# Optimization experiments

Measured on AMD Instinct MI355X. Metric: run time of the kernel, lower is better.

The kernel has to match this reference:

```python
import jax, jax.numpy as jnp
import numpy as np

EPS = 1e-7  # keras.backend.epsilon()
R_ITER = 3

def _squash(v, axis=-1):
    s2 = jnp.sum(jnp.square(v), axis=axis, keepdims=True)
    scale = s2 / (1.0 + s2) / jnp.sqrt(s2 + EPS)
    return scale * v

def setup_inputs() -> dict:
    key = jax.random.key(0)
    k1, k2 = jax.random.split(key)
    B, J, Din = 64, 2048, 16   # batch, input_n_capsules, input_dim_capsule
    C, Dout = 32, 32           # n_capsules, out_dim_capsule
    x = jax.random.normal(k1, (B, J, Din), dtype=jnp.float32)
    # glorot-uniform-like init for W [C, J, Dout, Din]
    limit = np.sqrt(6.0 / (Din + Dout)).astype(np.float32)
    W = jax.random.uniform(k2, (C, J, Dout, Din), dtype=jnp.float32, minval=-limit, maxval=limit)
    return {"x": x, "W": W}

def reference(x, W):
    # u_hat[b,c,j,o] = sum_i W[c,j,o,i] * x[b,j,i]
    u_hat = jnp.einsum('bji,cjoi->bcjo', x, W)
    B, C, J, _ = u_hat.shape
    b = jnp.zeros((B, C, J), dtype=u_hat.dtype)
    v = None
    for i in range(R_ITER):
        c = jax.nn.softmax(b, axis=1)               # softmax over output capsules (axis=1, as in source)
        s = jnp.einsum('bcj,bcjo->bco', c, u_hat)   # weighted sum over input capsules
        v = _squash(s, axis=-1)                     # [B, C, Dout]
        if i < R_ITER - 1:
            b = b + jnp.einsum('bco,bcjo->bcj', v, u_hat)
    return v
```

## Files before the change

kernel.cpp:

```cpp
#include <hip/hip_runtime.h>
#include <hip/hip_bf16.h>
#include <stdint.h>

#define BB 64
#define JJ 2048
#define DI 16
#define CC 32
#define OO 32
#define CO 1024
#define TJ 16
#define NJT 128

static const size_t W2_BYTES = (size_t)CC * JJ * OO * DI * 2;
static const size_t X3_BYTES = (size_t)BB * JJ * DI * 2;

typedef _Float16 f16x4 __attribute__((ext_vector_type(4)));
typedef float    f32x4 __attribute__((ext_vector_type(4)));
typedef unsigned short ushort_t;

#if defined(__HIP_DEVICE_COMPILE__)
# if __has_builtin(__builtin_amdgcn_mfma_f32_16x16x16f16)
#  define MFMA16(a, b, c) __builtin_amdgcn_mfma_f32_16x16x16f16((a), (b), (c), 0, 0, 0)
# else
#  define MFMA16(a, b, c) __builtin_amdgcn_mfma_f32_16x16x16_f16((a), (b), (c), 0, 0, 0)
# endif
# define SCHED_FENCE() __builtin_amdgcn_sched_barrier(0)
#else
# define MFMA16(a, b, c) (c)
# define SCHED_FENCE()
#endif

#if __has_attribute(amdgpu_waves_per_eu)
# define WAVES4 __attribute__((amdgpu_waves_per_eu(4, 4)))
#else
# define WAVES4
#endif

union Pack2 { unsigned u; _Float16 h[2]; };

__device__ __forceinline__ ushort_t f2bf(float f) {
  unsigned u = __float_as_uint(f);
  u += 0x7FFFu + ((u >> 16) & 1u);
  return (ushort_t)(u >> 16);
}
__device__ __forceinline__ float bf2f(ushort_t b) {
  return __uint_as_float(((unsigned)b) << 16);
}

__global__ __launch_bounds__(256) void prep_w(const float* __restrict__ W,
                                              uint2* __restrict__ W2) {
  const int j = blockIdx.x;
  const int tt = threadIdx.x;
#pragma unroll
  for (int r = 0; r < 16; ++r) {
    const int s = r * 256 + tt;
    const int ct = s >> 6, l = s & 63;
    const int co = ct * 16 + (l & 15);
    const int c = co >> 5, o = co & 31;
    const float4 src = ((const float4*)W)[(((size_t)c * JJ + j) * OO + o) * 4 + (l >> 4)];
    Pack2 a, b;
    a.h[0] = (_Float16)src.x; a.h[1] = (_Float16)src.y;
    b.h[0] = (_Float16)src.z; b.h[1] = (_Float16)src.w;
    W2[(size_t)j * 4096 + s] = make_uint2(a.u, b.u);
  }
}

__global__ __launch_bounds__(256) void prep_x(const float* __restrict__ X,
                                              uint2* __restrict__ X3) {
  const unsigned T = blockIdx.x * 256 + threadIdx.x;
  const int l = T & 63, bt = (T >> 6) & 1, j = (T >> 7) & 2047, bq = (int)(T >> 18);
  const int b = bq * 32 + bt * 16 + (l & 15);
  const float4 src = ((const float4*)X)[((size_t)b * JJ + j) * 4 + (l >> 4)];
  Pack2 a, bb;
  a.h[0] = (_Float16)src.x; a.h[1] = (_Float16)src.y;
  bb.h[0] = (_Float16)src.z; bb.h[1] = (_Float16)src.w;
  X3[T] = make_uint2(a.u, bb.u);
}

template<bool HAVE_V>
__global__ __launch_bounds__(1024, 4) WAVES4 void route_mfma(
    const uint4* __restrict__ X3, const uint4* __restrict__ W2,
    const float* __restrict__ vsum, ushort_t* __restrict__ partial)
{
  __shared__ uint4 wbuf[4][2048];
  __shared__ uint4 xbuf[1024];
  __shared__ float lbuf[2][32 * 33];

  const int jt   = blockIdx.x & (NJT - 1);
  const int bq   = blockIdx.x >> 7;
  const int tid  = threadIdx.x;
  const int w    = tid >> 6;
  const int lane = tid & 63;
  const int g    = lane >> 4;
  const int t    = lane & 15;

  unsigned vsh[2][2][2][2];
  if (HAVE_V) {
#pragma unroll
    for (int cc = 0; cc < 2; ++cc)
#pragma unroll
      for (int bt = 0; bt < 2; ++bt)
#pragma unroll
        for (int hh = 0; hh < 2; ++hh)
#pragma unroll
          for (int rp = 0; rp < 2; ++rp) {
            const float* vp = vsum + (size_t)(bq * 32 + bt * 16 + t) * CO
                            + (2 * w + cc) * OO + hh * 16 + 4 * g + 2 * rp;
            Pack2 p; p.h[0] = (_Float16)vp[0]; p.h[1] = (_Float16)vp[1];
            vsh[cc][bt][hh][rp] = p.u;
          }
    asm volatile("s_waitcnt vmcnt(0)" ::: "memory");
  }

  const uint4* wsrc = W2 + (size_t)jt * TJ * 2048;

#define STAGEW(bufidx, slab) do {                                                 \
    const uint4* sp_ = wsrc + (size_t)(slab) * 2048 + w * 128 + lane;             \
    uint4* dp_ = &wbuf[bufidx][w * 128 + lane];                                   \
    _Pragma("unroll")                                                             \
    for (int r_ = 0; r_ < 2; ++r_)                                                \
      __builtin_amdgcn_global_load_lds(                                           \
          (const __attribute__((address_space(1))) void*)(sp_ + r_ * 64),         \
          (__attribute__((address_space(3))) void*)(dp_ + r_ * 64), 16, 0, 0);    \
  } while (0)

  {
    const uint4* xs = X3 + ((size_t)bq * JJ + jt * TJ) * 64 + tid;
    __builtin_amdgcn_global_load_lds(
        (const __attribute__((address_space(1))) void*)xs,
        (__attribute__((address_space(3))) void*)&xbuf[tid], 16, 0, 0);
  }
  STAGEW(0, 0);
  STAGEW(1, 1);
  STAGEW(2, 2);
  asm volatile("s_waitcnt vmcnt(6)" ::: "memory");
  SCHED_FENCE();
  __builtin_amdgcn_s_barrier();

  f32x4 acc[4][2];
#pragma unroll
  for (int k = 0; k < 4; ++k)
#pragma unroll
    for (int bt = 0; bt < 2; ++bt) acc[k][bt] = f32x4{0.f, 0.f, 0.f, 0.f};

  for (int jj = 0; jj < TJ; ++jj) {
    const int bcur = jj & 3;
    if (jj < TJ - 2)       asm volatile("s_waitcnt vmcnt(4)" ::: "memory");
    else if (jj == TJ - 2) asm volatile("s_waitcnt vmcnt(2)" ::: "memory");
    else                   asm volatile("s_waitcnt vmcnt(0)" ::: "memory");
    SCHED_FENCE();
    if (jj + 3 < TJ) STAGEW((jj + 3) & 3, jj + 3);

    const uint2* wb2 = (const uint2*)wbuf[bcur];
    const uint2* xb2 = (const uint2*)xbuf;

    f16x4 bf[2];
#pragma unroll
    for (int bt = 0; bt < 2; ++bt)
      bf[bt] = __builtin_bit_cast(f16x4, xb2[(jj * 2 + bt) * 64 + lane]);
    f16x4 af[4];
#pragma unroll
    for (int k = 0; k < 4; ++k)
      af[k] = __builtin_bit_cast(f16x4, wb2[(w * 4 + k) * 64 + lane]);

    f32x4 uh[4][2];
#pragma unroll
    for (int k = 0; k < 4; ++k)
#pragma unroll
      for (int bt = 0; bt < 2; ++bt) {
        if (HAVE_V) uh[k][bt] = MFMA16(af[k], bf[bt], (f32x4{0.f, 0.f, 0.f, 0.f}));
        else        acc[k][bt] = MFMA16(af[k], bf[bt], acc[k][bt]);
      }

    if (HAVE_V) {
      float lp[2][2];
#pragma unroll
      for (int cc = 0; cc < 2; ++cc)
#pragma unroll
        for (int bt = 0; bt < 2; ++bt) {
          float s = 0.f;
#pragma unroll
          for (int hh = 0; hh < 2; ++hh)
#pragma unroll
            for (int rp = 0; rp < 2; ++rp) {
              Pack2 p; p.u = vsh[cc][bt][hh][rp];
              s = fmaf(uh[2 * cc + hh][bt][2 * rp],     (float)p.h[0], s);
              s = fmaf(uh[2 * cc + hh][bt][2 * rp + 1], (float)p.h[1], s);
            }
          s += __shfl_xor(s, 16);
          s += __shfl_xor(s, 32);
          lp[cc][bt] = s;
        }
      {
        const float hi = (g & 1) ? lp[1][1] : lp[1][0];
        const float lo = (g & 1) ? lp[0][1] : lp[0][0];
        const float val = (g >> 1) ? hi : lo;
        lbuf[jj & 1][((g & 1) * 16 + t) * 33 + 2 * w + (g >> 1)] = val;
      }
      asm volatile("s_waitcnt lgkmcnt(0)" ::: "memory");
      SCHED_FENCE();
      __builtin_amdgcn_s_barrier();

      {
        const int row = 2 * w + (lane >> 5);
        const int cc2 = lane & 31;
        float e = __expf(lbuf[jj & 1][row * 33 + cc2]);
        float den = e;
        den += __shfl_xor(den, 1);  den += __shfl_xor(den, 2);
        den += __shfl_xor(den, 4);  den += __shfl_xor(den, 8);
        den += __shfl_xor(den, 16);
        lbuf[jj & 1][row * 33 + cc2] = e / den;
      }
      asm volatile("s_waitcnt lgkmcnt(0)" ::: "memory");
      SCHED_FENCE();
      __builtin_amdgcn_s_barrier();

      float cf[2][2];
#pragma unroll
      for (int cc = 0; cc < 2; ++cc)
#pragma unroll
        for (int bt = 0; bt < 2; ++bt)
          cf[cc][bt] = lbuf[jj & 1][(bt * 16 + t) * 33 + 2 * w + cc];
#pragma unroll
      for (int k = 0; k < 4; ++k)
#pragma unroll
        for (int bt = 0; bt < 2; ++bt)
#pragma unroll
          for (int r = 0; r < 4; ++r)
            acc[k][bt][r] = fmaf(cf[k >> 1][bt], uh[k][bt][r], acc[k][bt][r]);
    }
  }
#undef STAGEW

  const float cs = HAVE_V ? 1.f : 0.03125f;
#pragma unroll
  for (int k = 0; k < 4; ++k)
#pragma unroll
    for (int bt = 0; bt < 2; ++bt) {
      const int b  = bq * 32 + bt * 16 + t;
      const int co = (4 * w + k) * 16 + 4 * g;
      ushort4 v;
      v.x = f2bf(acc[k][bt][0] * cs);
      v.y = f2bf(acc[k][bt][1] * cs);
      v.z = f2bf(acc[k][bt][2] * cs);
      v.w = f2bf(acc[k][bt][3] * cs);
      *(ushort4*)(partial + ((size_t)jt * BB + b) * CO + co) = v;
    }
}

template<bool HAVE_V>
__global__ __launch_bounds__(256, 1) void route_f32(
    const float* __restrict__ X, const float* __restrict__ W,
    const float* __restrict__ vsum, float* __restrict__ partial)
{
  const int jt   = blockIdx.x & 63;
  const int bq   = blockIdx.x >> 6;
  const int tid  = threadIdx.x;
  const int wave = tid >> 6;
  const int lane = tid & 63;
  const int c    = lane & 31;
  const int o0   = (lane >> 5) << 4;
  const int b0   = bq * 16 + wave * 4;

  float acc[4][16];
#pragma unroll
  for (int bl = 0; bl < 4; ++bl)
#pragma unroll
    for (int ol = 0; ol < 16; ++ol) acc[bl][ol] = 0.f;

  const float* wbase = W + ((size_t)c * JJ * OO + (size_t)o0) * DI;

  for (int jj = 0; jj < 32; ++jj) {
    const int j = jt * 32 + jj;
    float xf[4][16];
#pragma unroll
    for (int bl = 0; bl < 4; ++bl) {
      const float4* xpt = (const float4*)(X + ((size_t)(b0 + bl) * JJ + j) * DI);
#pragma unroll
      for (int q = 0; q < 4; ++q) {
        float4 x4 = xpt[q];
        xf[bl][4*q+0] = x4.x; xf[bl][4*q+1] = x4.y;
        xf[bl][4*q+2] = x4.z; xf[bl][4*q+3] = x4.w;
      }
    }
    const float4* wp = (const float4*)(wbase + (size_t)j * OO * DI);
    float tv[4][16];
#pragma unroll
    for (int ol = 0; ol < 16; ++ol) {
      float wf[16];
#pragma unroll
      for (int q = 0; q < 4; ++q) {
        float4 w4 = wp[4*ol + q];
        wf[4*q+0] = w4.x; wf[4*q+1] = w4.y;
        wf[4*q+2] = w4.z; wf[4*q+3] = w4.w;
      }
#pragma unroll
      for (int bl = 0; bl < 4; ++bl) {
        float tt = 0.f;
#pragma unroll
        for (int i = 0; i < 16; ++i) tt = fmaf(wf[i], xf[bl][i], tt);
        if (!HAVE_V) acc[bl][ol] += tt;
        else         tv[bl][ol] = tt;
      }
    }
    if (HAVE_V) {
#pragma unroll
      for (int bl = 0; bl < 4; ++bl) {
        float dsum = 0.f;
        const float4* vp = (const float4*)(vsum + (size_t)(b0 + bl) * CO + c * OO + o0);
#pragma unroll
        for (int q = 0; q < 4; ++q) {
          float4 v4 = vp[q];
          dsum = fmaf(v4.x, tv[bl][4*q+0], dsum);
          dsum = fmaf(v4.y, tv[bl][4*q+1], dsum);
          dsum = fmaf(v4.z, tv[bl][4*q+2], dsum);
          dsum = fmaf(v4.w, tv[bl][4*q+3], dsum);
        }
        dsum += __shfl_xor(dsum, 32);
        float mm = dsum;
#pragma unroll
        for (int s = 16; s >= 1; s >>= 1) mm = fmaxf(mm, __shfl_xor(mm, s));
        float e = __expf(dsum - mm);
        float den = e;
#pragma unroll
        for (int s = 16; s >= 1; s >>= 1) den += __shfl_xor(den, s);
        float coef = e / den;
#pragma unroll
        for (int ol = 0; ol < 16; ++ol)
          acc[bl][ol] = fmaf(coef, tv[bl][ol], acc[bl][ol]);
      }
    }
  }
  const float cs = HAVE_V ? 1.f : 0.03125f;
#pragma unroll
  for (int bl = 0; bl < 4; ++bl) {
    float* pp = partial + ((size_t)jt * BB + (b0 + bl)) * CO + c * OO + o0;
#pragma unroll
    for (int q = 0; q < 4; ++q) {
      float4 w4 = make_float4(acc[bl][4*q+0]*cs, acc[bl][4*q+1]*cs,
                              acc[bl][4*q+2]*cs, acc[bl][4*q+3]*cs);
      ((float4*)pp)[q] = w4;
    }
  }
}

__global__ __launch_bounds__(256, 1) void reduce_squash_bf(
    const ushort_t* __restrict__ partial, float* __restrict__ vsum,
    float* __restrict__ out, int mode)
{
  const int idx = blockIdx.x * 256 + threadIdx.x;
  float s0 = 0.f, s1 = 0.f, s2 = 0.f, s3 = 0.f;
#pragma unroll 4
  for (int nt = 0; nt < NJT; nt += 4) {
    s0 += bf2f(partial[(size_t)(nt + 0) * (BB * CO) + idx]);
    s1 += bf2f(partial[(size_t)(nt + 1) * (BB * CO) + idx]);
    s2 += bf2f(partial[(size_t)(nt + 2) * (BB * CO) + idx]);
    s3 += bf2f(partial[(size_t)(nt + 3) * (BB * CO) + idx]);
  }
  float s = (s0 + s1) + (s2 + s3);
  float s2m = s * s;
#pragma unroll
  for (int mk = 16; mk >= 1; mk >>= 1) s2m += __shfl_xor(s2m, mk);
  float scale = s2m / ((1.f + s2m) * sqrtf(s2m + 1e-7f));
  float v = scale * s;
  if (mode == 2)      out[idx] = v;
  else if (mode == 1) vsum[idx] += v;
  else                vsum[idx] = v;
}

template<int NJTR>
__global__ __launch_bounds__(256, 1) void reduce_squash(
    const float* __restrict__ partial, float* __restrict__ vsum,
    float* __restrict__ out, int mode)
{
  const int idx = blockIdx.x * 256 + threadIdx.x;
  float s0 = 0.f, s1 = 0.f, s2 = 0.f, s3 = 0.f;
#pragma unroll 4
  for (int nt = 0; nt < NJTR; nt += 4) {
    s0 += partial[(size_t)(nt + 0) * (BB * CO) + idx];
    s1 += partial[(size_t)(nt + 1) * (BB * CO) + idx];
    s2 += partial[(size_t)(nt + 2) * (BB * CO) + idx];
    s3 += partial[(size_t)(nt + 3) * (BB * CO) + idx];
  }
  float s = (s0 + s1) + (s2 + s3);
  float s2m = s * s;
#pragma unroll
  for (int mk = 16; mk >= 1; mk >>= 1) s2m += __shfl_xor(s2m, mk);
  float scale = s2m / ((1.f + s2m) * sqrtf(s2m + 1e-7f));
  float v = scale * s;
  if (mode == 2)      out[idx] = v;
  else if (mode == 1) vsum[idx] += v;
  else                vsum[idx] = v;
}

static void run_mfma(const float* X, const float* W, float* out,
                     void* d_ws, hipStream_t stream)
{
  uint2* W2         = (uint2*)d_ws;
  uint2* X3         = (uint2*)((char*)d_ws + W2_BYTES);
  ushort_t* partial = (ushort_t*)((char*)d_ws + W2_BYTES + X3_BYTES);
  float* vsum       = (float*)((char*)d_ws + W2_BYTES + X3_BYTES
                               + (size_t)NJT * BB * CO * 2);
  const int grid  = NJT * 2;
  const int rgrid = BB * CO / 256;

  prep_w<<<JJ, 256, 0, stream>>>(W, W2);
  prep_x<<<2048, 256, 0, stream>>>(X, X3);

  route_mfma<false><<<grid, 1024, 0, stream>>>((const uint4*)X3, (const uint4*)W2, nullptr, partial);
  reduce_squash_bf<<<rgrid, 256, 0, stream>>>(partial, vsum, nullptr, 0);

  route_mfma<true><<<grid, 1024, 0, stream>>>((const uint4*)X3, (const uint4*)W2, vsum, partial);
  reduce_squash_bf<<<rgrid, 256, 0, stream>>>(partial, vsum, nullptr, 1);

  route_mfma<true><<<grid, 1024, 0, stream>>>((const uint4*)X3, (const uint4*)W2, vsum, partial);
  reduce_squash_bf<<<rgrid, 256, 0, stream>>>(partial, vsum, out, 2);
}

static void run_f32_fallback(const float* X, const float* W, float* out,
                             void* d_ws, hipStream_t stream)
{
  float* partial = (float*)d_ws;
  float* vsum    = partial + (size_t)64 * BB * CO;
  const int grid  = 64 * 4;
  const int rgrid = BB * CO / 256;

  route_f32<false><<<grid, 256, 0, stream>>>(X, W, nullptr, partial);
  reduce_squash<64><<<rgrid, 256, 0, stream>>>(partial, vsum, nullptr, 0);
  route_f32<true><<<grid, 256, 0, stream>>>(X, W, vsum, partial);
  reduce_squash<64><<<rgrid, 256, 0, stream>>>(partial, vsum, nullptr, 1);
  route_f32<true><<<grid, 256, 0, stream>>>(X, W, vsum, partial);
  reduce_squash<64><<<rgrid, 256, 0, stream>>>(partial, vsum, out, 2);
}

extern "C" void kernel_launch(void* const* d_in, const int* in_sizes, int n_in,
                              void* d_out, int out_size, void* d_ws, size_t ws_size,
                              hipStream_t stream) {
  (void)in_sizes; (void)n_in; (void)out_size;
  const float* X = (const float*)d_in[0];
  const float* W = (const float*)d_in[1];
  float* out = (float*)d_out;

  const size_t need = W2_BYTES + X3_BYTES
                    + (size_t)NJT * BB * CO * 2 + (size_t)BB * CO * 4;
  if (ws_size >= need) run_mfma(X, W, out, d_ws, stream);
  else                 run_f32_fallback(X, W, out, d_ws, stream);
}
```

Before: 148.6 us.

## Fuse W fp16 conversion into first routing pass kernel

Drops the separate prep_w kernel. The first routing iteration now reads fp32 W directly into LDS, converts it to fp16 for the MFMA, and has the blocks with bq==0 write the converted W2 for the later iterations. This removes one full read of the fp32 W (about 134MB) and a kernel launch. In exchange the first pass stages double-size fp32 tiles with only two buffers, and the bq==1 blocks also read fp32 W.

After: 136.9 us. 1.09x faster.

```diff
diff --git a/kernel.cpp b/kernel.cpp
--- a/kernel.cpp
+++ b/kernel.cpp
@@ -47,24 +47,6 @@
   return __uint_as_float(((unsigned)b) << 16);
 }
 
-__global__ __launch_bounds__(256) void prep_w(const float* __restrict__ W,
-                                              uint2* __restrict__ W2) {
-  const int j = blockIdx.x;
-  const int tt = threadIdx.x;
-#pragma unroll
-  for (int r = 0; r < 16; ++r) {
-    const int s = r * 256 + tt;
-    const int ct = s >> 6, l = s & 63;
-    const int co = ct * 16 + (l & 15);
-    const int c = co >> 5, o = co & 31;
-    const float4 src = ((const float4*)W)[(((size_t)c * JJ + j) * OO + o) * 4 + (l >> 4)];
-    Pack2 a, b;
-    a.h[0] = (_Float16)src.x; a.h[1] = (_Float16)src.y;
-    b.h[0] = (_Float16)src.z; b.h[1] = (_Float16)src.w;
-    W2[(size_t)j * 4096 + s] = make_uint2(a.u, b.u);
-  }
-}
-
 __global__ __launch_bounds__(256) void prep_x(const float* __restrict__ X,
                                               uint2* __restrict__ X3) {
   const unsigned T = blockIdx.x * 256 + threadIdx.x;
@@ -77,14 +59,12 @@
   X3[T] = make_uint2(a.u, bb.u);
 }
 
-template<bool HAVE_V>
-__global__ __launch_bounds__(1024, 4) WAVES4 void route_mfma(
-    const uint4* __restrict__ X3, const uint4* __restrict__ W2,
-    const float* __restrict__ vsum, ushort_t* __restrict__ partial)
-{
-  __shared__ uint4 wbuf[4][2048];
+__global__ __launch_bounds__(1024, 4) WAVES4 void route_conv(
+    const uint4* __restrict__ X3, const float* __restrict__ Wf,
+    uint2* __restrict__ W2out, ushort_t* __restrict__ partial)
+{
+  __shared__ uint4 wbuf32[2][4096];
   __shared__ uint4 xbuf[1024];
-  __shared__ float lbuf[2][32 * 33];
 
   const int jt   = blockIdx.x & (NJT - 1);
   const int bq   = blockIdx.x >> 7;
@@ -94,23 +74,129 @@
   const int g    = lane >> 4;
   const int t    = lane & 15;
 
+#define STAGEC(slot, jjv) do {                                                    \
+    const int j_ = jt * TJ + (jjv);                                               \
+    _Pragma("unroll")                                                             \
+    for (int r_ = 0; r_ < 4; ++r_) {                                              \
+      const int ct_ = w * 4 + r_;                                                 \
+      const uint4* sp_ = (const uint4*)Wf                                         \
+          + ((size_t)(ct_ >> 1) * JJ + j_) * 128 + (ct_ & 1) * 64                 \
+          + (lane & 15) * 4 + (lane >> 4);                                        \
+      uint4* dp_ = &wbuf32[slot][w * 256 + r_ * 64 + lane];                       \
+      __builtin_amdgcn_global_load_lds(                                           \
+          (const __attribute__((address_space(1))) void*)sp_,                     \
+          (__attribute__((address_space(3))) void*)dp_, 16, 0, 0);                \
+    }                                                                             \
+  } while (0)
+
+  {
+    const uint4* xs = X3 + ((size_t)bq * JJ + jt * TJ) * 64 + tid;
+    __builtin_amdgcn_global_load_lds(
+        (const __attribute__((address_space(1))) void*)xs,
+        (__attribute__((address_space(3))) void*)&xbuf[tid], 16, 0, 0);
+  }
+  STAGEC(0, 0);
+  STAGEC(1, 1);
+  asm volatile("s_waitcnt vmcnt(8)" ::: "memory");
+  SCHED_FENCE();
+  __builtin_amdgcn_s_barrier();
+
+  f32x4 acc[4][2];
+#pragma unroll
+  for (int k = 0; k < 4; ++k)
+#pragma unroll
+    for (int bt = 0; bt < 2; ++bt) acc[k][bt] = f32x4{0.f, 0.f, 0.f, 0.f};
+
+  for (int jj = 0; jj < TJ; ++jj) {
+    const int bcur = jj & 1;
+    if (jj < TJ - 2) asm volatile("s_waitcnt vmcnt(4)" ::: "memory");
+    else             asm volatile("s_waitcnt vmcnt(0)" ::: "memory");
+    SCHED_FENCE();
+
+    const uint2* xb2 = (const uint2*)xbuf;
+    f16x4 bf[2];
+#pragma unroll
+    for (int bt = 0; bt < 2; ++bt)
+      bf[bt] = __builtin_bit_cast(f16x4, xb2[(jj * 2 + bt) * 64 + lane]);
+
+    const f32x4* wr = (const f32x4*)wbuf32[bcur];
+    f16x4 af[4];
+#pragma unroll
+    for (int k = 0; k < 4; ++k) {
+      f32x4 a32 = wr[w * 256 + k * 64 + lane];
+      af[k][0] = (_Float16)a32[0]; af[k][1] = (_Float16)a32[1];
+      af[k][2] = (_Float16)a32[2]; af[k][3] = (_Float16)a32[3];
+    }
+
+    if (bq == 0) {
+      const size_t wbase = (size_t)(jt * TJ + jj) * 4096;
+#pragma unroll
+      for (int k = 0; k < 4; ++k) {
+        Pack2 p0, p1;
+        p0.h[0] = af[k][0]; p0.h[1] = af[k][1];
+        p1.h[0] = af[k][2]; p1.h[1] = af[k][3];
+        W2out[wbase + (w * 4 + k) * 64 + lane] = make_uint2(p0.u, p1.u);
+      }
+    }
+
+#pragma unroll
+    for (int k = 0; k < 4; ++k)
+#pragma unroll
+      for (int bt = 0; bt < 2; ++bt)
+        acc[k][bt] = MFMA16(af[k], bf[bt], acc[k][bt]);
+
+    asm volatile("s_waitcnt lgkmcnt(0)" ::: "memory");
+    SCHED_FENCE();
+    if (jj + 2 < TJ) STAGEC(bcur, jj + 2);
+  }
+#undef STAGEC
+
+#pragma unroll
+  for (int k = 0; k < 4; ++k)
+#pragma unroll
+    for (int bt = 0; bt < 2; ++bt) {
+      const int b  = bq * 32 + bt * 16 + t;
+      const int co = (4 * w + k) * 16 + 4 * g;
+      ushort4 v;
+      v.x = f2bf(acc[k][bt][0] * 0.03125f);
+      v.y = f2bf(acc[k][bt][1] * 0.03125f);
+      v.z = f2bf(acc[k][bt][2] * 0.03125f);
+      v.w = f2bf(acc[k][bt][3] * 0.03125f);
+      *(ushort4*)(partial + ((size_t)jt * BB + b) * CO + co) = v;
+    }
+}
+
+__global__ __launch_bounds__(1024, 4) WAVES4 void route_v(
+    const uint4* __restrict__ X3, const uint4* __restrict__ W2,
+    const float* __restrict__ vsum, ushort_t* __restrict__ partial)
+{
+  __shared__ uint4 wbuf[4][2048];
+  __shared__ uint4 xbuf[1024];
+  __shared__ float lbuf[2][32 * 33];
+
+  const int jt   = blockIdx.x & (NJT - 1);
+  const int bq   = blockIdx.x >> 7;
+  const int tid  = threadIdx.x;
+  const int w    = tid >> 6;
+  const int lane = tid & 63;
+  const int g    = lane >> 4;
+  const int t    = lane & 15;
+
   unsigned vsh[2][2][2][2];
-  if (HAVE_V) {
-#pragma unroll
-    for (int cc = 0; cc < 2; ++cc)
-#pragma unroll
-      for (int bt = 0; bt < 2; ++bt)
-#pragma unroll
-        for (int hh = 0; hh < 2; ++hh)
-#pragma unroll
-          for (int rp = 0; rp < 2; ++rp) {
-            const float* vp = vsum + (size_t)(bq * 32 + bt * 16 + t) * CO
-                            + (2 * w + cc) * OO + hh * 16 + 4 * g + 2 * rp;
-            Pack2 p; p.h[0] = (_Float16)vp[0]; p.h[1] = (_Float16)vp[1];
-            vsh[cc][bt][hh][rp] = p.u;
-          }
-    asm volatile("s_waitcnt vmcnt(0)" ::: "memory");
-  }
+#pragma unroll
+  for (int cc = 0; cc < 2; ++cc)
+#pragma unroll
+    for (int bt = 0; bt < 2; ++bt)
+#pragma unroll
+      for (int hh = 0; hh < 2; ++hh)
+#pragma unroll
+        for (int rp = 0; rp < 2; ++rp) {
+          const float* vp = vsum + (size_t)(bq * 32 + bt * 16 + t) * CO
+                          + (2 * w + cc) * OO + hh * 16 + 4 * g + 2 * rp;
+          Pack2 p; p.h[0] = (_Float16)vp[0]; p.h[1] = (_Float16)vp[1];
+          vsh[cc][bt][hh][rp] = p.u;
+        }
+  asm volatile("s_waitcnt vmcnt(0)" ::: "memory");
 
   const uint4* wsrc = W2 + (size_t)jt * TJ * 2048;
 
@@ -167,72 +253,67 @@
 #pragma unroll
     for (int k = 0; k < 4; ++k)
 #pragma unroll
+      for (int bt = 0; bt < 2; ++bt)
+        uh[k][bt] = MFMA16(af[k], bf[bt], (f32x4{0.f, 0.f, 0.f, 0.f}));
+
+    float lp[2][2];
+#pragma unroll
+    for (int cc = 0; cc < 2; ++cc)
+#pragma unroll
       for (int bt = 0; bt < 2; ++bt) {
-        if (HAVE_V) uh[k][bt] = MFMA16(af[k], bf[bt], (f32x4{0.f, 0.f, 0.f, 0.f}));
-        else        acc[k][bt] = MFMA16(af[k], bf[bt], acc[k][bt]);
+        float s = 0.f;
+#pragma unroll
+        for (int hh = 0; hh < 2; ++hh)
+#pragma unroll
+          for (int rp = 0; rp < 2; ++rp) {
+            Pack2 p; p.u = vsh[cc][bt][hh][rp];
+            s = fmaf(uh[2 * cc + hh][bt][2 * rp],     (float)p.h[0], s);
+            s = fmaf(uh[2 * cc + hh][bt][2 * rp + 1], (float)p.h[1], s);
+          }
+        s += __shfl_xor(s, 16);
+        s += __shfl_xor(s, 32);
+        lp[cc][bt] = s;
       }
-
-    if (HAVE_V) {
-      float lp[2][2];
-#pragma unroll
-      for (int cc = 0; cc < 2; ++cc)
-#pragma unroll
-        for (int bt = 0; bt < 2; ++bt) {
-          float s = 0.f;
-#pragma unroll
-          for (int hh = 0; hh < 2; ++hh)
-#pragma unroll
-            for (int rp = 0; rp < 2; ++rp) {
-              Pack2 p; p.u = vsh[cc][bt][hh][rp];
-              s = fmaf(uh[2 * cc + hh][bt][2 * rp],     (float)p.h[0], s);
-              s = fmaf(uh[2 * cc + hh][bt][2 * rp + 1], (float)p.h[1], s);
-            }
-          s += __shfl_xor(s, 16);
-          s += __shfl_xor(s, 32);
-          lp[cc][bt] = s;
-        }
-      {
-        const float hi = (g & 1) ? lp[1][1] : lp[1][0];
-        const float lo = (g & 1) ? lp[0][1] : lp[0][0];
-        const float val = (g >> 1) ? hi : lo;
-        lbuf[jj & 1][((g & 1) * 16 + t) * 33 + 2 * w + (g >> 1)] = val;
-      }
-      asm volatile("s_waitcnt lgkmcnt(0)" ::: "memory");
-      SCHED_FENCE();
-      __builtin_amdgcn_s_barrier();
-
-      {
-        const int row = 2 * w + (lane >> 5);
-        const int cc2 = lane & 31;
-        float e = __expf(lbuf[jj & 1][row * 33 + cc2]);
-        float den = e;
-        den += __shfl_xor(den, 1);  den += __shfl_xor(den, 2);
-        den += __shfl_xor(den, 4);  den += __shfl_xor(den, 8);
-        den += __shfl_xor(den, 16);
-        lbuf[jj & 1][row * 33 + cc2] = e / den;
-      }
-      asm volatile("s_waitcnt lgkmcnt(0)" ::: "memory");
-      SCHED_FENCE();
-      __builtin_amdgcn_s_barrier();
-
-      float cf[2][2];
-#pragma unroll
-      for (int cc = 0; cc < 2; ++cc)
-#pragma unroll
-        for (int bt = 0; bt < 2; ++bt)
-          cf[cc][bt] = lbuf[jj & 1][(bt * 16 + t) * 33 + 2 * w + cc];
-#pragma unroll
-      for (int k = 0; k < 4; ++k)
-#pragma unroll
-        for (int bt = 0; bt < 2; ++bt)
-#pragma unroll
-          for (int r = 0; r < 4; ++r)
-            acc[k][bt][r] = fmaf(cf[k >> 1][bt], uh[k][bt][r], acc[k][bt][r]);
-    }
+    {
+      const float hi = (g & 1) ? lp[1][1] : lp[1][0];
+      const float lo = (g & 1) ? lp[0][1] : lp[0][0];
+      const float val = (g >> 1) ? hi : lo;
+      lbuf[jj & 1][((g & 1) * 16 + t) * 33 + 2 * w + (g >> 1)] = val;
+    }
+    asm volatile("s_waitcnt lgkmcnt(0)" ::: "memory");
+    SCHED_FENCE();
+    __builtin_amdgcn_s_barrier();
+
+    {
+      const int row = 2 * w + (lane >> 5);
+      const int cc2 = lane & 31;
+      float e = __expf(lbuf[jj & 1][row * 33 + cc2]);
+      float den = e;
+      den += __shfl_xor(den, 1);  den += __shfl_xor(den, 2);
+      den += __shfl_xor(den, 4);  den += __shfl_xor(den, 8);
+      den += __shfl_xor(den, 16);
+      lbuf[jj & 1][row * 33 + cc2] = e / den;
+    }
+    asm volatile("s_waitcnt lgkmcnt(0)" ::: "memory");
+    SCHED_FENCE();
+    __builtin_amdgcn_s_barrier();
+
+    float cf[2][2];
+#pragma unroll
+    for (int cc = 0; cc < 2; ++cc)
+#pragma unroll
+      for (int bt = 0; bt < 2; ++bt)
+        cf[cc][bt] = lbuf[jj & 1][(bt * 16 + t) * 33 + 2 * w + cc];
+#pragma unroll
+    for (int k = 0; k < 4; ++k)
+#pragma unroll
+      for (int bt = 0; bt < 2; ++bt)
+#pragma unroll
+        for (int r = 0; r < 4; ++r)
+          acc[k][bt][r] = fmaf(cf[k >> 1][bt], uh[k][bt][r], acc[k][bt][r]);
   }
 #undef STAGEW
 
-  const float cs = HAVE_V ? 1.f : 0.03125f;
 #pragma unroll
   for (int k = 0; k < 4; ++k)
 #pragma unroll
@@ -240,10 +321,10 @@
       const int b  = bq * 32 + bt * 16 + t;
       const int co = (4 * w + k) * 16 + 4 * g;
       ushort4 v;
-      v.x = f2bf(acc[k][bt][0] * cs);
-      v.y = f2bf(acc[k][bt][1] * cs);
-      v.z = f2bf(acc[k][bt][2] * cs);
-      v.w = f2bf(acc[k][bt][3] * cs);
+      v.x = f2bf(acc[k][bt][0]);
+      v.y = f2bf(acc[k][bt][1]);
+      v.z = f2bf(acc[k][bt][2]);
+      v.w = f2bf(acc[k][bt][3]);
       *(ushort4*)(partial + ((size_t)jt * BB + b) * CO + co) = v;
     }
 }
@@ -404,16 +485,15 @@
   const int grid  = NJT * 2;
   const int rgrid = BB * CO / 256;
 
-  prep_w<<<JJ, 256, 0, stream>>>(W, W2);
   prep_x<<<2048, 256, 0, stream>>>(X, X3);
 
-  route_mfma<false><<<grid, 1024, 0, stream>>>((const uint4*)X3, (const uint4*)W2, nullptr, partial);
+  route_conv<<<grid, 1024, 0, stream>>>((const uint4*)X3, W, W2, partial);
   reduce_squash_bf<<<rgrid, 256, 0, stream>>>(partial, vsum, nullptr, 0);
 
-  route_mfma<true><<<grid, 1024, 0, stream>>>((const uint4*)X3, (const uint4*)W2, vsum, partial);
+  route_v<<<grid, 1024, 0, stream>>>((const uint4*)X3, (const uint4*)W2, vsum, partial);
   reduce_squash_bf<<<rgrid, 256, 0, stream>>>(partial, vsum, nullptr, 1);
 
-  route_mfma<true><<<grid, 1024, 0, stream>>>((const uint4*)X3, (const uint4*)W2, vsum, partial);
+  route_v<<<grid, 1024, 0, stream>>>((const uint4*)X3, (const uint4*)W2, vsum, partial);
   reduce_squash_bf<<<rgrid, 256, 0, stream>>>(partial, vsum, out, 2);
 }
 
```
